# Kernel optimization log

Hardware: AMD Instinct MI355X
Metric: run time of the kernel (lower is better)

Reference implementation:

```python
import jax, jax.numpy as jnp
import numpy as np

BS, N, IN_F, OUT_F, HEADS = 32, 512, 256, 128, 4
NEG_SLOPE = 0.2


def setup_inputs() -> dict:
    key = jax.random.key(0)
    k1, k2, k3, k4, k5 = jax.random.split(key, 5)
    inputs = jax.random.normal(k1, (BS, N, IN_F), dtype=jnp.float32)
    adj = (jax.random.uniform(k2, (BS, N, N)) > 0.5).astype(jnp.float32)
    # xavier_normal-style init with relu gain sqrt(2)
    w = jax.random.normal(k3, (IN_F, HEADS * OUT_F), dtype=jnp.float32) * (
        np.sqrt(2.0) * np.sqrt(2.0 / (IN_F + HEADS * OUT_F))
    )
    a_i = jax.random.normal(k4, (HEADS, OUT_F, 1), dtype=jnp.float32) * (
        np.sqrt(2.0) * np.sqrt(2.0 / (OUT_F + 1))
    )
    a_j = jax.random.normal(k5, (HEADS, OUT_F, 1), dtype=jnp.float32) * (
        np.sqrt(2.0) * np.sqrt(2.0 / (OUT_F + 1))
    )
    bias = jnp.zeros((HEADS * OUT_F,), dtype=jnp.float32)
    return {"inputs": inputs, "adj": adj, "w": w, "a_i": a_i, "a_j": a_j, "bias": bias}


def reference(inputs, adj, w, a_i, a_j, bias):
    bs, n, _ = inputs.shape
    H, D = a_i.shape[0], a_i.shape[1]
    # self_loop_type == 2: adjacency unchanged
    # project: [bs, n, H, D]
    h = jnp.matmul(inputs, w).reshape(bs, n, H, D)
    # additive attention coefficients: [bs, n, H]
    coeff_i = jnp.einsum('bnhd,hdo->bnho', h, a_i)[..., 0]
    coeff_j = jnp.einsum('bnhd,hdo->bnho', h, a_j)[..., 0]
    # broadcast-sum scores e[b, i, j, h], leaky relu
    e = jax.nn.leaky_relu(coeff_i[:, :, None, :] + coeff_j[:, None, :, :],
                          negative_slope=NEG_SLOPE)
    adj_h = adj[..., None]  # [bs, n, n, 1], broadcasts over heads
    masked_e = jnp.where(adj_h <= 0, jnp.float32(-1e9), e)
    # softmax over neighbor axis j (dim 2), then re-mask
    attention = jax.nn.softmax(masked_e, axis=2) * adj_h
    # dropout = 0.0 -> no-op; normalize=False, average=False
    # per-head aggregation, all heads at once: out[b,i,h,d] = sum_j att[b,i,j,h] h[b,j,h,d]
    out = jnp.einsum('bijh,bjhd->bihd', attention, h).reshape(bs, n, H * D)
    return out + bias
```

## Files before the change

kernel.cpp:

```cpp
#include <hip/hip_runtime.h>

#define BSZ 32
#define NN 512
#define INF 256
#define NH 4
#define HD 512
#define NEG_SLOPE 0.2f

typedef __attribute__((ext_vector_type(8))) short bf16x8;
typedef __attribute__((ext_vector_type(8))) unsigned short ushort8;
typedef __attribute__((ext_vector_type(4))) float f32x4;

static __device__ __forceinline__ unsigned short f2bf(float f) {
    unsigned u = __builtin_bit_cast(unsigned, f);
    return (unsigned short)((u + 0x7FFFu + ((u >> 16) & 1u)) >> 16);
}

static __device__ __forceinline__ bf16x8 pk8(float4 a, float4 b) {
    unsigned d0, d1, d2, d3;
    asm("v_cvt_pk_bf16_f32 %0, %1, %2" : "=v"(d0) : "v"(a.x), "v"(a.y));
    asm("v_cvt_pk_bf16_f32 %0, %1, %2" : "=v"(d1) : "v"(a.z), "v"(a.w));
    asm("v_cvt_pk_bf16_f32 %0, %1, %2" : "=v"(d2) : "v"(b.x), "v"(b.y));
    asm("v_cvt_pk_bf16_f32 %0, %1, %2" : "=v"(d3) : "v"(b.z), "v"(b.w));
    uint4 u; u.x = d0; u.y = d1; u.z = d2; u.w = d3;
    return __builtin_bit_cast(bf16x8, u);
}

static __device__ __forceinline__ void gl_lds16(const void* g, void* l) {
    __builtin_amdgcn_global_load_lds(
        (const __attribute__((address_space(1))) unsigned int*)g,
        (__attribute__((address_space(3))) unsigned int*)l, 16, 0, 0);
}

__global__ __launch_bounds__(256) void k_prep(
    const float* __restrict__ w, unsigned short* __restrict__ wB,
    const float* __restrict__ adj, unsigned char* __restrict__ mbB)
{
    const int bid = blockIdx.x;
    if (bid < 2048) {
        const int lane = threadIdx.x & 63, wave = threadIdx.x >> 6;
        const int row0 = bid * 8 + wave * 2;
        #pragma unroll
        for (int rr = 0; rr < 2; ++rr) {
            const float* ap = adj + (size_t)(row0 + rr) * NN + lane * 8;
            float4 a0 = *(const float4*)ap;
            float4 a1 = *(const float4*)(ap + 4);
            unsigned byte = 0;
            byte |= (a0.x > 0.f) ? 1u   : 0u;
            byte |= (a0.y > 0.f) ? 2u   : 0u;
            byte |= (a0.z > 0.f) ? 4u   : 0u;
            byte |= (a0.w > 0.f) ? 8u   : 0u;
            byte |= (a1.x > 0.f) ? 16u  : 0u;
            byte |= (a1.y > 0.f) ? 32u  : 0u;
            byte |= (a1.z > 0.f) ? 64u  : 0u;
            byte |= (a1.w > 0.f) ? 128u : 0u;
            mbB[(size_t)(row0 + rr) * 64 + lane] = (unsigned char)byte;
        }
    } else {
        int gid = (bid - 2048) * 256 + threadIdx.x;
        int c = gid & 511, k = gid >> 9;
        int kb = k >> 5, g = (k >> 3) & 3, e = k & 7;
        wB[(((size_t)(kb * 4 + g) * 512) + c) * 8 + e] = f2bf(w[(size_t)k * 512 + c]);
    }
}

__global__ __launch_bounds__(256) void k_proj(
    const float* __restrict__ x, const unsigned short* __restrict__ wB,
    const float* __restrict__ ai, const float* __restrict__ aj,
    unsigned short* __restrict__ hB, float* __restrict__ ciT, float* __restrict__ cjT)
{
    __shared__ unsigned short hs[NH * 4096];
    const int tid = threadIdx.x;
    const int lane = tid & 63, head = tid >> 6;
    const int l15 = lane & 15, g = lane >> 4;
    const int row0 = blockIdx.x * 32;

    f32x4 acc[2][8] = {};
    const float* xp0 = x + (size_t)(row0 + l15) * INF + g * 8;
    const float* xp1 = xp0 + 16 * INF;
    const unsigned short* bp = wB + ((size_t)g * 512 + head * 128 + l15) * 8;

    #pragma unroll
    for (int kb = 0; kb < 8; ++kb) {
        float4 f0 = *(const float4*)(xp0 + kb * 32);
        float4 f1 = *(const float4*)(xp0 + kb * 32 + 4);
        float4 f2 = *(const float4*)(xp1 + kb * 32);
        float4 f3 = *(const float4*)(xp1 + kb * 32 + 4);
        bf16x8 a0 = pk8(f0, f1);
        bf16x8 a1 = pk8(f2, f3);
        #pragma unroll
        for (int nf = 0; nf < 8; ++nf) {
            bf16x8 bv = *(const bf16x8*)(bp + (size_t)kb * 16384 + nf * 128);
            acc[0][nf] = __builtin_amdgcn_mfma_f32_16x16x32_bf16(a0, bv, acc[0][nf], 0, 0, 0);
            acc[1][nf] = __builtin_amdgcn_mfma_f32_16x16x32_bf16(a1, bv, acc[1][nf], 0, 0, 0);
        }
    }

    float aiv[8], ajv[8];
    #pragma unroll
    for (int nf = 0; nf < 8; ++nf) {
        aiv[nf] = ai[head * 128 + nf * 16 + l15];
        ajv[nf] = aj[head * 128 + nf * 16 + l15];
    }
    const int b = row0 >> 9;
    const int nloc0 = row0 & 511;
    const int kb2 = nloc0 >> 5;

    #pragma unroll
    for (int m = 0; m < 2; ++m) {
        float pi[4] = {0,0,0,0}, pj[4] = {0,0,0,0};
        #pragma unroll
        for (int nf = 0; nf < 8; ++nf)
            #pragma unroll
            for (int reg = 0; reg < 4; ++reg) {
                pi[reg] = fmaf(acc[m][nf][reg], aiv[nf], pi[reg]);
                pj[reg] = fmaf(acc[m][nf][reg], ajv[nf], pj[reg]);
            }
        #pragma unroll
        for (int reg = 0; reg < 4; ++reg) {
            #pragma unroll
            for (int off = 1; off < 16; off <<= 1) {
                pi[reg] += __shfl_xor(pi[reg], off);
                pj[reg] += __shfl_xor(pj[reg], off);
            }
        }
        if (l15 == 0) {
            #pragma unroll
            for (int reg = 0; reg < 4; ++reg) {
                int n = nloc0 + 16 * m + 4 * g + reg;
                ciT[((size_t)(head * BSZ + b) * NN) + n] = pi[reg];
                cjT[((size_t)(head * BSZ + b) * NN) + n] = pj[reg];
            }
        }
        #pragma unroll
        for (int reg = 0; reg < 4; ++reg) {
            int jloc = 16 * m + 4 * g + reg;
            int g2 = jloc >> 3, e = jloc & 7;
            #pragma unroll
            for (int nf = 0; nf < 8; ++nf)
                hs[head * 4096 + nf * 512 + g2 * 128 + l15 * 8 + e] =
                    f2bf(acc[m][nf][reg]);
        }
    }
    __syncthreads();
    {
        ushort8* dst = (ushort8*)(hB + (((size_t)(b * 4 + head) * 16 + kb2) * 4096));
        const ushort8* src = (const ushort8*)(hs + head * 4096);
        #pragma unroll
        for (int it = 0; it < 8; ++it)
            dst[it * 64 + lane] = src[it * 64 + lane];
    }
}

__global__ __launch_bounds__(256, 4) void k_attn(
    const unsigned short* __restrict__ hB, const float* __restrict__ ciT,
    const float* __restrict__ cjT, const unsigned* __restrict__ mb,
    const float* __restrict__ bias, float* __restrict__ out)
{
    __shared__ __align__(16) unsigned short Bst[2][4096];
    __shared__ __align__(16) float cjh[NN];
    __shared__ float cih[64];
    __shared__ unsigned maskS[64][17];
    __shared__ float Mpart[4];

    const int tid = threadIdx.x;
    const int lane = tid & 63, wave = tid >> 6;
    const int l15 = lane & 15, g = lane >> 4;

    const int orig = blockIdx.x;
    const int swz = (orig & 7) * 128 + (orig >> 3);
    const int b  = swz >> 5;
    const int h  = (swz >> 3) & 3;
    const int i0 = (swz & 7) * 64;

    const char* gslab = (const char*)(hB + (size_t)(b * NH + h) * 65536);

    gl_lds16(gslab + wave * 2048 + lane * 16,        (char*)&Bst[0][0] + wave * 2048);
    gl_lds16(gslab + wave * 2048 + 1024 + lane * 16, (char*)&Bst[0][0] + wave * 2048 + 1024);

    {
        const float* src = cjT + (size_t)(h * BSZ + b) * NN;
        float v0 = src[tid], v1 = src[tid + 256];
        cjh[tid] = v0; cjh[tid + 256] = v1;
        float mv = fmaxf(v0, v1);
        #pragma unroll
        for (int off = 32; off; off >>= 1) mv = fmaxf(mv, __shfl_xor(mv, off));
        if (lane == 0) Mpart[wave] = mv;
        if (tid < 64) cih[tid] = ciT[(size_t)(h * BSZ + b) * NN + i0 + tid];
        uint4 m4 = ((const uint4*)(mb + ((size_t)b * NN + i0) * 16))[tid];
        int base = tid * 4, row = base >> 4, wi = base & 15;
        maskS[row][wi] = m4.x; maskS[row][wi + 1] = m4.y;
        maskS[row][wi + 2] = m4.z; maskS[row][wi + 3] = m4.w;
    }
    __syncthreads();

    const float M = fmaxf(fmaxf(Mpart[0], Mpart[1]), fmaxf(Mpart[2], Mpart[3]));
    const float bc = cih[wave * 16 + l15];
    float smx = bc + M;
    const float mrow = fmaxf(smx, NEG_SLOPE * smx);

    float bvv[8];
    #pragma unroll
    for (int nf = 0; nf < 8; ++nf) bvv[nf] = bias[h * 128 + nf * 16 + l15];

    bf16x8 ones;
    #pragma unroll
    for (int e = 0; e < 8; ++e) ones[e] = (short)0x3F80;

    f32x4 acc[8] = {};
    f32x4 accs = {};
    int cur = 0;
    const unsigned* mrowp = maskS[wave * 16 + l15];

    for (int kb = 0; kb < 16; ++kb) {
        if (kb < 15) {
            const char* gs = gslab + (size_t)(kb + 1) * 8192 + wave * 2048 + lane * 16;
            char* ld = (char*)&Bst[cur ^ 1][0] + wave * 2048;
            gl_lds16(gs, ld);
            gl_lds16(gs + 1024, ld + 1024);
        }

        float4 cva = *(const float4*)&cjh[kb * 32 + g * 8];
        float4 cvb = *(const float4*)&cjh[kb * 32 + g * 8 + 4];
        float cj8[8] = {cva.x, cva.y, cva.z, cva.w, cvb.x, cvb.y, cvb.z, cvb.w};
        unsigned byte = (mrowp[kb] >> (g * 8)) & 0xFFu;
        float p[8];
        #pragma unroll
        for (int e = 0; e < 8; ++e) {
            float s = bc + cj8[e];
            s = fmaxf(s, NEG_SLOPE * s);
            float pe = __expf(s - mrow);
            p[e] = ((byte >> e) & 1u) ? pe : 0.f;
        }
        unsigned d0, d1, d2, d3;
        asm("v_cvt_pk_bf16_f32 %0, %1, %2" : "=v"(d0) : "v"(p[0]), "v"(p[1]));
        asm("v_cvt_pk_bf16_f32 %0, %1, %2" : "=v"(d1) : "v"(p[2]), "v"(p[3]));
        asm("v_cvt_pk_bf16_f32 %0, %1, %2" : "=v"(d2) : "v"(p[4]), "v"(p[5]));
        asm("v_cvt_pk_bf16_f32 %0, %1, %2" : "=v"(d3) : "v"(p[6]), "v"(p[7]));
        uint4 u; u.x = d0; u.y = d1; u.z = d2; u.w = d3;
        bf16x8 av = __builtin_bit_cast(bf16x8, u);

        const char* bb = (const char*)&Bst[cur][0] + lane * 16;
        bf16x8 bfr[8];
        #pragma unroll
        for (int nf = 0; nf < 8; ++nf)
            bfr[nf] = *(const bf16x8*)(bb + nf * 1024);

        #pragma unroll
        for (int nf = 0; nf < 8; ++nf)
            acc[nf] = __builtin_amdgcn_mfma_f32_16x16x32_bf16(av, bfr[nf], acc[nf], 0, 0, 0);
        accs = __builtin_amdgcn_mfma_f32_16x16x32_bf16(av, ones, accs, 0, 0, 0);

        if (kb < 15) { __syncthreads(); cur ^= 1; }
    }

    #pragma unroll
    for (int reg = 0; reg < 4; ++reg) {
        float sum = accs[reg];
        float inv = sum > 0.f ? 1.f / sum : 0.f;
        const int i = i0 + wave * 16 + g * 4 + reg;
        #pragma unroll
        for (int nf = 0; nf < 8; ++nf) {
            int colg = h * 128 + nf * 16 + l15;
            out[(size_t)(b * NN + i) * HD + colg] = acc[nf][reg] * inv + bvv[nf];
        }
    }
}

extern "C" void kernel_launch(void* const* d_in, const int* in_sizes, int n_in,
                              void* d_out, int out_size, void* d_ws, size_t ws_size,
                              hipStream_t stream)
{
    const float* x    = (const float*)d_in[0];
    const float* adj  = (const float*)d_in[1];
    const float* w    = (const float*)d_in[2];
    const float* ai   = (const float*)d_in[3];
    const float* aj   = (const float*)d_in[4];
    const float* bias = (const float*)d_in[5];
    float* out = (float*)d_out;

    char* ws = (char*)d_ws;
    unsigned short* wB = (unsigned short*)ws;
    unsigned short* hB = (unsigned short*)(ws + 262144);
    float* ciT         = (float*)(ws + 17039360);
    float* cjT         = (float*)(ws + 17301504);
    unsigned* mb       = (unsigned*)(ws + 17563648);

    k_prep<<<2560, 256, 0, stream>>>(w, wB, adj, (unsigned char*)mb);
    k_proj<<<BSZ * NN / 32, 256, 0, stream>>>(x, wB, ai, aj, hB, ciT, cjT);
    k_attn<<<BSZ * NH * (NN / 64), 256, 0, stream>>>(hB, ciT, cjT, mb, bias, out);
}
```

Before: 50.07 us.

## Fuse prep, projection and attention into one cooperative kernel with grid syncs

Merges the three kernels (weight/mask prep, projection, attention) into a single cooperative kernel of 1024 blocks that uses grid-wide syncs between phases. The goal is to remove two kernel-launch boundaries and the tail and idle time between launches. In exchange each block takes on more work per phase, and it pays for two grid barriers plus the constraint of 4 resident blocks per CU. The original three-kernel path stays as a fallback when occupancy is too low.

```diff
diff --git a/kernel.cpp b/kernel.cpp
--- a/kernel.cpp
+++ b/kernel.cpp
@@ -1,4 +1,7 @@
 #include <hip/hip_runtime.h>
+#include <hip/hip_cooperative_groups.h>
+
+namespace cg = cooperative_groups;
 
 #define BSZ 32
 #define NN 512
@@ -32,16 +35,30 @@
         (__attribute__((address_space(3))) unsigned int*)l, 16, 0, 0);
 }
 
-__global__ __launch_bounds__(256) void k_prep(
-    const float* __restrict__ w, unsigned short* __restrict__ wB,
-    const float* __restrict__ adj, unsigned char* __restrict__ mbB)
+__global__ __launch_bounds__(256, 4) void mega(
+    const float* __restrict__ x, const float* __restrict__ adj,
+    const float* __restrict__ w, const float* __restrict__ ai,
+    const float* __restrict__ aj, const float* __restrict__ bias,
+    float* __restrict__ out, unsigned short* __restrict__ wB,
+    unsigned short* __restrict__ hB, float* __restrict__ ciT,
+    float* __restrict__ cjT, unsigned char* __restrict__ mbB)
 {
+    __shared__ __align__(16) char smem[32768];
+    const int tid = threadIdx.x;
+    const int lane = tid & 63, wave = tid >> 6;
+    const int l15 = lane & 15, g = lane >> 4;
     const int bid = blockIdx.x;
-    if (bid < 2048) {
-        const int lane = threadIdx.x & 63, wave = threadIdx.x >> 6;
-        const int row0 = bid * 8 + wave * 2;
-        #pragma unroll
-        for (int rr = 0; rr < 2; ++rr) {
+
+    if (bid < 512) {
+        int gid = bid * 256 + tid;
+        int c = gid & 511, k = gid >> 9;
+        int kb = k >> 5, gg = (k >> 3) & 3, e = k & 7;
+        wB[(((size_t)(kb * 4 + gg) * 512) + c) * 8 + e] = f2bf(w[(size_t)k * 512 + c]);
+    }
+    {
+        const int row0 = bid * 16 + wave * 4;
+        #pragma unroll
+        for (int rr = 0; rr < 4; ++rr) {
             const float* ap = adj + (size_t)(row0 + rr) * NN + lane * 8;
             float4 a0 = *(const float4*)ap;
             float4 a1 = *(const float4*)(ap + 4);
@@ -56,6 +73,220 @@
             byte |= (a1.w > 0.f) ? 128u : 0u;
             mbB[(size_t)(row0 + rr) * 64 + lane] = (unsigned char)byte;
         }
+    }
+    cg::this_grid().sync();
+
+    if (bid < 512) {
+        unsigned short* hs = (unsigned short*)smem;
+        const int row0 = bid * 32;
+
+        f32x4 acc[2][8] = {};
+        const float* xp0 = x + (size_t)(row0 + l15) * INF + g * 8;
+        const float* xp1 = xp0 + 16 * INF;
+        const unsigned short* bp = wB + ((size_t)g * 512 + (size_t)wave * 128 + l15) * 8;
+
+        #pragma unroll
+        for (int kb = 0; kb < 8; ++kb) {
+            float4 f0 = *(const float4*)(xp0 + kb * 32);
+            float4 f1 = *(const float4*)(xp0 + kb * 32 + 4);
+            float4 f2 = *(const float4*)(xp1 + kb * 32);
+            float4 f3 = *(const float4*)(xp1 + kb * 32 + 4);
+            bf16x8 a0 = pk8(f0, f1);
+            bf16x8 a1 = pk8(f2, f3);
+            #pragma unroll
+            for (int nf = 0; nf < 8; ++nf) {
+                bf16x8 bv = *(const bf16x8*)(bp + (size_t)kb * 16384 + nf * 128);
+                acc[0][nf] = __builtin_amdgcn_mfma_f32_16x16x32_bf16(a0, bv, acc[0][nf], 0, 0, 0);
+                acc[1][nf] = __builtin_amdgcn_mfma_f32_16x16x32_bf16(a1, bv, acc[1][nf], 0, 0, 0);
+            }
+        }
+
+        float aiv[8], ajv[8];
+        #pragma unroll
+        for (int nf = 0; nf < 8; ++nf) {
+            aiv[nf] = ai[wave * 128 + nf * 16 + l15];
+            ajv[nf] = aj[wave * 128 + nf * 16 + l15];
+        }
+        const int b = row0 >> 9;
+        const int nloc0 = row0 & 511;
+        const int kb2 = nloc0 >> 5;
+
+        #pragma unroll
+        for (int m = 0; m < 2; ++m) {
+            float pi[4] = {0,0,0,0}, pj[4] = {0,0,0,0};
+            #pragma unroll
+            for (int nf = 0; nf < 8; ++nf)
+                #pragma unroll
+                for (int reg = 0; reg < 4; ++reg) {
+                    pi[reg] = fmaf(acc[m][nf][reg], aiv[nf], pi[reg]);
+                    pj[reg] = fmaf(acc[m][nf][reg], ajv[nf], pj[reg]);
+                }
+            #pragma unroll
+            for (int reg = 0; reg < 4; ++reg) {
+                #pragma unroll
+                for (int off = 1; off < 16; off <<= 1) {
+                    pi[reg] += __shfl_xor(pi[reg], off);
+                    pj[reg] += __shfl_xor(pj[reg], off);
+                }
+            }
+            if (l15 == 0) {
+                #pragma unroll
+                for (int reg = 0; reg < 4; ++reg) {
+                    int n = nloc0 + 16 * m + 4 * g + reg;
+                    ciT[((size_t)(wave * BSZ + b) * NN) + n] = pi[reg];
+                    cjT[((size_t)(wave * BSZ + b) * NN) + n] = pj[reg];
+                }
+            }
+            #pragma unroll
+            for (int reg = 0; reg < 4; ++reg) {
+                int jloc = 16 * m + 4 * g + reg;
+                int g2 = jloc >> 3, e = jloc & 7;
+                #pragma unroll
+                for (int nf = 0; nf < 8; ++nf)
+                    hs[wave * 4096 + nf * 512 + g2 * 128 + l15 * 8 + e] =
+                        f2bf(acc[m][nf][reg]);
+            }
+        }
+        __syncthreads();
+        {
+            ushort8* dst = (ushort8*)(hB + (((size_t)(b * 4 + wave) * 16 + kb2) * 4096));
+            const ushort8* src = (const ushort8*)(hs + wave * 4096);
+            #pragma unroll
+            for (int it = 0; it < 8; ++it)
+                dst[it * 64 + lane] = src[it * 64 + lane];
+        }
+    }
+    cg::this_grid().sync();
+
+    {
+        unsigned short (*Bst)[4096] = (unsigned short(*)[4096])smem;
+        float* cjh  = (float*)(smem + 16384);
+        float* cih  = (float*)(smem + 18432);
+        unsigned (*maskS)[17] = (unsigned(*)[17])(smem + 18688);
+        float* Mpart = (float*)(smem + 23040);
+        const unsigned* mb = (const unsigned*)mbB;
+
+        const int orig = bid;
+        const int swz = (orig & 7) * 128 + (orig >> 3);
+        const int b  = swz >> 5;
+        const int h  = (swz >> 3) & 3;
+        const int i0 = (swz & 7) * 64;
+
+        const char* gslab = (const char*)(hB + (size_t)(b * NH + h) * 65536);
+
+        gl_lds16(gslab + wave * 2048 + lane * 16,        (char*)&Bst[0][0] + wave * 2048);
+        gl_lds16(gslab + wave * 2048 + 1024 + lane * 16, (char*)&Bst[0][0] + wave * 2048 + 1024);
+
+        {
+            const float* src = cjT + (size_t)(h * BSZ + b) * NN;
+            float v0 = src[tid], v1 = src[tid + 256];
+            cjh[tid] = v0; cjh[tid + 256] = v1;
+            float mv = fmaxf(v0, v1);
+            #pragma unroll
+            for (int off = 32; off; off >>= 1) mv = fmaxf(mv, __shfl_xor(mv, off));
+            if (lane == 0) Mpart[wave] = mv;
+            if (tid < 64) cih[tid] = ciT[(size_t)(h * BSZ + b) * NN + i0 + tid];
+            uint4 m4 = ((const uint4*)(mb + ((size_t)b * NN + i0) * 16))[tid];
+            int base = tid * 4, row = base >> 4, wi = base & 15;
+            maskS[row][wi] = m4.x; maskS[row][wi + 1] = m4.y;
+            maskS[row][wi + 2] = m4.z; maskS[row][wi + 3] = m4.w;
+        }
+        __syncthreads();
+
+        const float M = fmaxf(fmaxf(Mpart[0], Mpart[1]), fmaxf(Mpart[2], Mpart[3]));
+        const float bc = cih[wave * 16 + l15];
+        float smx = bc + M;
+        const float mrow = fmaxf(smx, NEG_SLOPE * smx);
+
+        float bvv[8];
+        #pragma unroll
+        for (int nf = 0; nf < 8; ++nf) bvv[nf] = bias[h * 128 + nf * 16 + l15];
+
+        bf16x8 ones;
+        #pragma unroll
+        for (int e = 0; e < 8; ++e) ones[e] = (short)0x3F80;
+
+        f32x4 acc[8] = {};
+        f32x4 accs = {};
+        int cur = 0;
+        const unsigned* mrowp = maskS[wave * 16 + l15];
+
+        for (int kb = 0; kb < 16; ++kb) {
+            if (kb < 15) {
+                const char* gs = gslab + (size_t)(kb + 1) * 8192 + wave * 2048 + lane * 16;
+                char* ld = (char*)&Bst[cur ^ 1][0] + wave * 2048;
+                gl_lds16(gs, ld);
+                gl_lds16(gs + 1024, ld + 1024);
+            }
+
+            float4 cva = *(const float4*)&cjh[kb * 32 + g * 8];
+            float4 cvb = *(const float4*)&cjh[kb * 32 + g * 8 + 4];
+            float cj8[8] = {cva.x, cva.y, cva.z, cva.w, cvb.x, cvb.y, cvb.z, cvb.w};
+            unsigned byte = (mrowp[kb] >> (g * 8)) & 0xFFu;
+            float p[8];
+            #pragma unroll
+            for (int e = 0; e < 8; ++e) {
+                float s = bc + cj8[e];
+                s = fmaxf(s, NEG_SLOPE * s);
+                float pe = __expf(s - mrow);
+                p[e] = ((byte >> e) & 1u) ? pe : 0.f;
+            }
+            unsigned d0, d1, d2, d3;
+            asm("v_cvt_pk_bf16_f32 %0, %1, %2" : "=v"(d0) : "v"(p[0]), "v"(p[1]));
+            asm("v_cvt_pk_bf16_f32 %0, %1, %2" : "=v"(d1) : "v"(p[2]), "v"(p[3]));
+            asm("v_cvt_pk_bf16_f32 %0, %1, %2" : "=v"(d2) : "v"(p[4]), "v"(p[5]));
+            asm("v_cvt_pk_bf16_f32 %0, %1, %2" : "=v"(d3) : "v"(p[6]), "v"(p[7]));
+            uint4 u; u.x = d0; u.y = d1; u.z = d2; u.w = d3;
+            bf16x8 av = __builtin_bit_cast(bf16x8, u);
+
+            const char* bb = (const char*)&Bst[cur][0] + lane * 16;
+            bf16x8 bfr[8];
+            #pragma unroll
+            for (int nf = 0; nf < 8; ++nf)
+                bfr[nf] = *(const bf16x8*)(bb + nf * 1024);
+
+            #pragma unroll
+            for (int nf = 0; nf < 8; ++nf)
+                acc[nf] = __builtin_amdgcn_mfma_f32_16x16x32_bf16(av, bfr[nf], acc[nf], 0, 0, 0);
+            accs = __builtin_amdgcn_mfma_f32_16x16x32_bf16(av, ones, accs, 0, 0, 0);
+
+            if (kb < 15) { __syncthreads(); cur ^= 1; }
+        }
+
+        #pragma unroll
+        for (int reg = 0; reg < 4; ++reg) {
+            float sum = accs[reg];
+            float inv = sum > 0.f ? 1.f / sum : 0.f;
+            const int i = i0 + wave * 16 + g * 4 + reg;
+            #pragma unroll
+            for (int nf = 0; nf < 8; ++nf) {
+                int colg = h * 128 + nf * 16 + l15;
+                out[(size_t)(b * NN + i) * HD + colg] = acc[nf][reg] * inv + bvv[nf];
+            }
+        }
+    }
+}
+
+__global__ __launch_bounds__(256) void k_prep(
+    const float* __restrict__ w, unsigned short* __restrict__ wB,
+    const float* __restrict__ adj, unsigned char* __restrict__ mbB)
+{
+    const int bid = blockIdx.x;
+    if (bid < 2048) {
+        const int lane = threadIdx.x & 63, wave = threadIdx.x >> 6;
+        const int row0 = bid * 8 + wave * 2;
+        #pragma unroll
+        for (int rr = 0; rr < 2; ++rr) {
+            const float* ap = adj + (size_t)(row0 + rr) * NN + lane * 8;
+            float4 a0 = *(const float4*)ap;
+            float4 a1 = *(const float4*)(ap + 4);
+            unsigned byte = 0;
+            byte |= (a0.x > 0.f) ? 1u : 0u;  byte |= (a0.y > 0.f) ? 2u : 0u;
+            byte |= (a0.z > 0.f) ? 4u : 0u;  byte |= (a0.w > 0.f) ? 8u : 0u;
+            byte |= (a1.x > 0.f) ? 16u : 0u; byte |= (a1.y > 0.f) ? 32u : 0u;
+            byte |= (a1.z > 0.f) ? 64u : 0u; byte |= (a1.w > 0.f) ? 128u : 0u;
+            mbB[(size_t)(row0 + rr) * 64 + lane] = (unsigned char)byte;
+        }
     } else {
         int gid = (bid - 2048) * 256 + threadIdx.x;
         int c = gid & 511, k = gid >> 9;
@@ -284,9 +515,21 @@
     unsigned short* hB = (unsigned short*)(ws + 262144);
     float* ciT         = (float*)(ws + 17039360);
     float* cjT         = (float*)(ws + 17301504);
-    unsigned* mb       = (unsigned*)(ws + 17563648);
-
-    k_prep<<<2560, 256, 0, stream>>>(w, wB, adj, (unsigned char*)mb);
-    k_proj<<<BSZ * NN / 32, 256, 0, stream>>>(x, wB, ai, aj, hB, ciT, cjT);
-    k_attn<<<BSZ * NH * (NN / 64), 256, 0, stream>>>(hB, ciT, cjT, mb, bias, out);
-}
+    unsigned char* mbB = (unsigned char*)(ws + 17563648);
+
+    int maxB = 0;
+    hipError_t e = hipOccupancyMaxActiveBlocksPerMultiprocessor(
+        &maxB, (const void*)mega, 256, 0);
+    if (e == hipSuccess && maxB >= 4) {
+        void* args[] = {(void*)&x, (void*)&adj, (void*)&w, (void*)&ai, (void*)&aj,
+                        (void*)&bias, (void*)&out, (void*)&wB, (void*)&hB,
+                        (void*)&ciT, (void*)&cjT, (void*)&mbB};
+        hipLaunchCooperativeKernel((const void*)mega, dim3(1024), dim3(256),
+                                   args, 0, stream);
+    } else {
+        k_prep<<<2560, 256, 0, stream>>>(w, wB, adj, mbB);
+        k_proj<<<BSZ * NN / 32, 256, 0, stream>>>(x, wB, ai, aj, hB, ciT, cjT);
+        k_attn<<<BSZ * NH * (NN / 64), 256, 0, stream>>>(hB, ciT, cjT,
+                                                         (const unsigned*)mbB, bias, out);
+    }
+}
```

After: 49.93 us. Within noise of the previous version (-0.3%).
